# Kernel tuning notes

Hardware: AMD Instinct MI355X
Metric: run time of the kernel (lower is better)

Reference implementation:

```python
import jax, jax.numpy as jnp
import numpy as np
from jax import lax

DIVISOR = 2.0
POOL = 2

def setup_inputs() -> dict:
    key = jax.random.key(0)
    k1, k2, k3, k4 = jax.random.split(key, 4)
    x = jax.random.normal(k1, (16, 8, 16, 128, 128), dtype=jnp.float32)
    conv_weight = jax.random.normal(k2, (32, 8, 3, 3, 3), dtype=jnp.float32) * 0.05
    conv_bias = jax.random.normal(k3, (32,), dtype=jnp.float32) * 0.05
    bias = jax.random.normal(k4, (32, 1, 1, 1), dtype=jnp.float32)
    return {"x": x, "conv_weight": conv_weight, "conv_bias": conv_bias, "bias": bias}

def reference(x, conv_weight, conv_bias, bias):
    # Conv3d, valid padding, stride 1: [B,Cin,D,H,W] -> [B,Cout,D-2,H-2,W-2]
    y = lax.conv_general_dilated(
        x, conv_weight,
        window_strides=(1, 1, 1), padding="VALID",
        dimension_numbers=("NCDHW", "OIDHW", "NCDHW"))
    y = y + conv_bias[None, :, None, None, None]
    y = y / DIVISOR
    # MaxPool3d(2): non-overlapping 2x2x2 windows, floor mode
    y = lax.reduce_window(
        y, -jnp.inf, lax.max,
        window_dimensions=(1, 1, POOL, POOL, POOL),
        window_strides=(1, 1, POOL, POOL, POOL),
        padding="VALID")
    # AdaptiveAvgPool3d((1,1,1)) -> [B,C,1,1,1]
    y = jnp.mean(y, axis=(2, 3, 4), keepdims=True)
    # bias add (C,1,1,1) then sum over channel dim (sum_dim=1)
    y = y + bias
    return jnp.sum(y, axis=1)  # [B,1,1,1]
```

## Files before the change

kernel.cpp:

```cpp
#include <hip/hip_runtime.h>
#include <math.h>

namespace {

constexpr int B = 16, CIN = 8, D = 16, H = 128, W = 128;
constexpr int PW = 63;
constexpr float INV_CNT = 1.0f / 27783.0f;
constexpr int HW = H * W, DHW = D * HW;

typedef short v8s  __attribute__((ext_vector_type(8)));
typedef float v16f __attribute__((ext_vector_type(16)));

constexpr int WB_OFF = 131072;
constexpr int RED_OFF = WB_OFF + 14336;
constexpr int LDS_BYTES = RED_OFF + 64;

__device__ inline unsigned short f2bf(float f) {
    unsigned int x = __builtin_bit_cast(unsigned int, f);
    return (unsigned short)((x + 0x7FFFu + ((x >> 16) & 1u)) >> 16);
}

__global__ __launch_bounds__(512, 2) void conv_mfma_kernel(
    const float* __restrict__ x,
    const float* __restrict__ wgt,
    const float* __restrict__ cbias,
    float* __restrict__ partials)
{
    __shared__ __align__(16) char smem[LDS_BYTES];

    const int bid = blockIdx.x;
    const int logical = (bid & 7) * 126 + (bid >> 3);
    const int ph = logical % 63;
    const int b  = logical / 63;

    const int t = threadIdx.x, lane = t & 63, wv = t >> 6;

    for (int pr = t; pr < 14 * 64; pr += 512) {
        const int p = pr >> 6, l = pr & 63;
        const int tap = 2 * p + (l >> 5), cout = l & 31;
        uint4 pk = {0u, 0u, 0u, 0u};
        if (tap < 27) {
            unsigned int v[4];
            #pragma unroll
            for (int j = 0; j < 4; ++j) {
                unsigned short b0 = f2bf(wgt[(cout * CIN + 2 * j) * 27 + tap]);
                unsigned short b1 = f2bf(wgt[(cout * CIN + 2 * j + 1) * 27 + tap]);
                v[j] = (unsigned int)b0 | ((unsigned int)b1 << 16);
            }
            pk = uint4{v[0], v[1], v[2], v[3]};
        }
        *reinterpret_cast<uint4*>(smem + WB_OFF + pr * 16) = pk;
    }

    const float* xb = x + (size_t)b * CIN * DHW;
    #pragma unroll 4
    for (int s = t; s < 8192; s += 512) {
        const int d = s >> 9, h = (s >> 7) & 3, w = s & 127;
        const float* xp = xb + d * HW + (2 * ph + h) * W + w;
        unsigned int v[4];
        #pragma unroll
        for (int j = 0; j < 4; ++j) {
            unsigned short b0 = f2bf(xp[(2 * j) * DHW]);
            unsigned short b1 = f2bf(xp[(2 * j + 1) * DHW]);
            v[j] = (unsigned int)b0 | ((unsigned int)b1 << 16);
        }
        const int byte = (s * 16) ^ ((h & 1) << 6);
        *reinterpret_cast<uint4*>(smem + byte) = uint4{v[0], v[1], v[2], v[3]};
    }

    __syncthreads();

    v8s Bf[14];
    #pragma unroll
    for (int ks = 0; ks < 14; ++ks)
        Bf[ks] = *reinterpret_cast<const v8s*>(smem + WB_OFF + (ks * 64 + lane) * 16);

    const int r = lane & 31, half = lane >> 5;
    const int hh = r >> 4, pwl = (r >> 1) & 7, ww = r & 1;
    const int wbase = 2 * (8 * wv + pwl) + ww;

    int offA[14];
    #pragma unroll
    for (int ks = 0; ks < 14; ++ks) {
        const int t0 = 2 * ks, t1 = t0 + 1;
        const int KD0 = t0 / 9, KH0 = (t0 % 9) / 3, KW0 = t0 % 3;
        const int KD1 = (t1 < 27) ? t1 / 9 : 0;
        const int KH1 = (t1 < 27) ? (t1 % 9) / 3 : 0;
        const int KW1 = (t1 < 27) ? t1 % 3 : 0;
        const int kd = half ? KD1 : KD0;
        const int kh = half ? KH1 : KH0;
        const int kw = half ? KW1 : KW0;
        const int h = hh + kh;
        int w = wbase + kw; w = (w > 127) ? 127 : w;
        offA[ks] = (((kd * 4 + h) * 128 + w) * 16) ^ ((h & 1) << 6);
    }

    const float cb = cbias[lane & 31];
    float lsum = 0.f;

    #pragma unroll 1
    for (int pd = 0; pd < 7; ++pd) {
        v16f acc0, acc1;
        #pragma unroll
        for (int i = 0; i < 16; ++i) { acc0[i] = 0.f; acc1[i] = 0.f; }
        const int pbase = pd * 16384;

        #pragma unroll
        for (int ks = 0; ks < 14; ++ks) {
            const v8s A0 = *reinterpret_cast<const v8s*>(smem + pbase + offA[ks]);
            const v8s A1 = *reinterpret_cast<const v8s*>(smem + pbase + offA[ks] + 8192);
            acc0 = __builtin_amdgcn_mfma_f32_32x32x16_bf16(A0, Bf[ks], acc0, 0, 0, 0);
            acc1 = __builtin_amdgcn_mfma_f32_32x32x16_bf16(A1, Bf[ks], acc1, 0, 0, 0);
        }

        #pragma unroll
        for (int j = 0; j < 4; ++j) {
            float m = fmaxf(fmaxf(acc0[2 * j], acc0[2 * j + 1]),
                            fmaxf(acc0[8 + 2 * j], acc0[9 + 2 * j]));
            m = fmaxf(m, fmaxf(fmaxf(acc1[2 * j], acc1[2 * j + 1]),
                               fmaxf(acc1[8 + 2 * j], acc1[9 + 2 * j])));
            const int pw = 8 * wv + ((j & 1) + ((j >> 1) << 2) + 2 * half);
            if (pw < PW) lsum += (m + cb) * 0.5f;
        }
    }

    #pragma unroll
    for (int o = 32; o > 0; o >>= 1) lsum += __shfl_xor(lsum, o, 64);
    if (lane == 0) *reinterpret_cast<float*>(smem + RED_OFF + wv * 4) = lsum;
    __syncthreads();
    if (t == 0) {
        float s = 0.f;
        #pragma unroll
        for (int i = 0; i < 8; ++i) s += reinterpret_cast<float*>(smem + RED_OFF)[i];
        partials[logical] = s;
    }
}

__global__ void finalize_kernel(const float* __restrict__ partials,
                                const float* __restrict__ bias,
                                float* __restrict__ out)
{
    const int t = threadIdx.x;
    const int b = t >> 5, l = t & 31;
    float s = 0.f;
    for (int j = l; j < 63; j += 32) s += partials[b * 63 + j];
    s = s * INV_CNT + bias[l];
    #pragma unroll
    for (int o = 16; o > 0; o >>= 1) s += __shfl_xor(s, o, 32);
    if (l == 0) out[b] = s;
}

}

extern "C" void kernel_launch(void* const* d_in, const int* in_sizes, int n_in,
                              void* d_out, int out_size, void* d_ws, size_t ws_size,
                              hipStream_t stream) {
    const float* x     = (const float*)d_in[0];
    const float* wgt   = (const float*)d_in[1];
    const float* cbias = (const float*)d_in[2];
    const float* bias  = (const float*)d_in[3];
    float* out      = (float*)d_out;
    float* partials = (float*)d_ws;

    hipLaunchKernelGGL(conv_mfma_kernel, dim3(B * 63), dim3(512), 0, stream,
                       x, wgt, cbias, partials);
    hipLaunchKernelGGL(finalize_kernel, dim3(1), dim3(512), 0, stream,
                       partials, bias, out);
}
```

Baseline: 242.9 us.

## Split depth pairs across waves and overlap input staging with MFMA compute

Each wave pair now splits the two depth slices of a pooled output row, and the conv tile is remapped so each wave covers a 32-wide w strip. Partial maxima are exchanged through a double-buffered LDS area. Only the first six input planes are staged before compute starts; the remaining planes are staged two at a time inside the depth loop, so global loads overlap with MFMA work. This drops the XOR swizzle and adds a block barrier per iteration, which may bring back LDS bank conflicts and synchronisation cost.

```diff
diff --git a/kernel.cpp b/kernel.cpp
--- a/kernel.cpp
+++ b/kernel.cpp
@@ -4,20 +4,37 @@
 namespace {
 
 constexpr int B = 16, CIN = 8, D = 16, H = 128, W = 128;
-constexpr int PW = 63;
 constexpr float INV_CNT = 1.0f / 27783.0f;
 constexpr int HW = H * W, DHW = D * HW;
 
 typedef short v8s  __attribute__((ext_vector_type(8)));
 typedef float v16f __attribute__((ext_vector_type(16)));
 
-constexpr int WB_OFF = 131072;
-constexpr int RED_OFF = WB_OFF + 14336;
+constexpr int WB_OFF  = 131072;
+constexpr int PM_OFF  = WB_OFF + 14336;
+constexpr int RED_OFF = PM_OFF + 16384;
 constexpr int LDS_BYTES = RED_OFF + 64;
 
 __device__ inline unsigned short f2bf(float f) {
     unsigned int x = __builtin_bit_cast(unsigned int, f);
     return (unsigned short)((x + 0x7FFFu + ((x >> 16) & 1u)) >> 16);
+}
+
+__device__ inline void stage_planes(char* smem, const float* xb, int ph,
+                                    int dlo, int nplanes, int t) {
+    for (int s = t; s < nplanes * 512; s += 512) {
+        const int d = dlo + (s >> 9), h = (s >> 7) & 3, w = s & 127;
+        const float* xp = xb + d * HW + (2 * ph + h) * W + w;
+        unsigned int v[4];
+        #pragma unroll
+        for (int j = 0; j < 4; ++j) {
+            unsigned short b0 = f2bf(xp[(2 * j) * DHW]);
+            unsigned short b1 = f2bf(xp[(2 * j + 1) * DHW]);
+            v[j] = (unsigned int)b0 | ((unsigned int)b1 << 16);
+        }
+        *reinterpret_cast<uint4*>(smem + ((d * 4 + h) * 128 + w) * 16) =
+            uint4{v[0], v[1], v[2], v[3]};
+    }
 }
 
 __global__ __launch_bounds__(512, 2) void conv_mfma_kernel(
@@ -34,6 +51,8 @@
     const int b  = logical / 63;
 
     const int t = threadIdx.x, lane = t & 63, wv = t >> 6;
+    const int dd = wv & 1, q = wv >> 1, w0 = 32 * q;
+    const int r = lane & 31, half = lane >> 5;
 
     for (int pr = t; pr < 14 * 64; pr += 512) {
         const int p = pr >> 6, l = pr & 63;
@@ -53,21 +72,7 @@
     }
 
     const float* xb = x + (size_t)b * CIN * DHW;
-    #pragma unroll 4
-    for (int s = t; s < 8192; s += 512) {
-        const int d = s >> 9, h = (s >> 7) & 3, w = s & 127;
-        const float* xp = xb + d * HW + (2 * ph + h) * W + w;
-        unsigned int v[4];
-        #pragma unroll
-        for (int j = 0; j < 4; ++j) {
-            unsigned short b0 = f2bf(xp[(2 * j) * DHW]);
-            unsigned short b1 = f2bf(xp[(2 * j + 1) * DHW]);
-            v[j] = (unsigned int)b0 | ((unsigned int)b1 << 16);
-        }
-        const int byte = (s * 16) ^ ((h & 1) << 6);
-        *reinterpret_cast<uint4*>(smem + byte) = uint4{v[0], v[1], v[2], v[3]};
-    }
-
+    stage_planes(smem, xb, ph, 0, 6, t);
     __syncthreads();
 
     v8s Bf[14];
@@ -75,24 +80,12 @@
     for (int ks = 0; ks < 14; ++ks)
         Bf[ks] = *reinterpret_cast<const v8s*>(smem + WB_OFF + (ks * 64 + lane) * 16);
 
-    const int r = lane & 31, half = lane >> 5;
-    const int hh = r >> 4, pwl = (r >> 1) & 7, ww = r & 1;
-    const int wbase = 2 * (8 * wv + pwl) + ww;
-
     int offA[14];
     #pragma unroll
     for (int ks = 0; ks < 14; ++ks) {
-        const int t0 = 2 * ks, t1 = t0 + 1;
-        const int KD0 = t0 / 9, KH0 = (t0 % 9) / 3, KW0 = t0 % 3;
-        const int KD1 = (t1 < 27) ? t1 / 9 : 0;
-        const int KH1 = (t1 < 27) ? (t1 % 9) / 3 : 0;
-        const int KW1 = (t1 < 27) ? t1 % 3 : 0;
-        const int kd = half ? KD1 : KD0;
-        const int kh = half ? KH1 : KH0;
-        const int kw = half ? KW1 : KW0;
-        const int h = hh + kh;
-        int w = wbase + kw; w = (w > 127) ? 127 : w;
-        offA[ks] = (((kd * 4 + h) * 128 + w) * 16) ^ ((h & 1) << 6);
+        int tap = 2 * ks + half; if (tap > 26) tap = 26;
+        const int kd = tap / 9, kh = (tap % 9) / 3, kw = tap % 3;
+        offA[ks] = kd * 8192 + kh * 2048 + (w0 + r + kw) * 16;
     }
 
     const float cb = cbias[lane & 31];
@@ -103,35 +96,52 @@
         v16f acc0, acc1;
         #pragma unroll
         for (int i = 0; i < 16; ++i) { acc0[i] = 0.f; acc1[i] = 0.f; }
-        const int pbase = pd * 16384;
+        const int cbase = (2 * pd + dd) * 8192;
 
         #pragma unroll
         for (int ks = 0; ks < 14; ++ks) {
-            const v8s A0 = *reinterpret_cast<const v8s*>(smem + pbase + offA[ks]);
-            const v8s A1 = *reinterpret_cast<const v8s*>(smem + pbase + offA[ks] + 8192);
+            const v8s A0 = *reinterpret_cast<const v8s*>(smem + cbase + offA[ks]);
+            const v8s A1 = *reinterpret_cast<const v8s*>(smem + cbase + offA[ks] + 2048);
             acc0 = __builtin_amdgcn_mfma_f32_32x32x16_bf16(A0, Bf[ks], acc0, 0, 0, 0);
             acc1 = __builtin_amdgcn_mfma_f32_32x32x16_bf16(A1, Bf[ks], acc1, 0, 0, 0);
         }
 
+        float pm[8];
         #pragma unroll
-        for (int j = 0; j < 4; ++j) {
-            float m = fmaxf(fmaxf(acc0[2 * j], acc0[2 * j + 1]),
-                            fmaxf(acc0[8 + 2 * j], acc0[9 + 2 * j]));
-            m = fmaxf(m, fmaxf(fmaxf(acc1[2 * j], acc1[2 * j + 1]),
-                               fmaxf(acc1[8 + 2 * j], acc1[9 + 2 * j])));
-            const int pw = 8 * wv + ((j & 1) + ((j >> 1) << 2) + 2 * half);
-            if (pw < PW) lsum += (m + cb) * 0.5f;
+        for (int i = 0; i < 8; ++i)
+            pm[i] = fmaxf(fmaxf(acc0[2 * i], acc0[2 * i + 1]),
+                          fmaxf(acc1[2 * i], acc1[2 * i + 1]));
+
+        char* pmbuf = smem + PM_OFF + (pd & 1) * 8192 + (q * 64 + lane) * 32;
+        if (dd == 1) {
+            *reinterpret_cast<float4*>(pmbuf)      = float4{pm[0], pm[1], pm[2], pm[3]};
+            *reinterpret_cast<float4*>(pmbuf + 16) = float4{pm[4], pm[5], pm[6], pm[7]};
+        }
+        if (pd <= 4) stage_planes(smem, xb, ph, 2 * pd + 6, 2, t);
+        __syncthreads();
+
+        if (dd == 0) {
+            const float4 pa = *reinterpret_cast<const float4*>(pmbuf);
+            const float4 pb = *reinterpret_cast<const float4*>(pmbuf + 16);
+            const float pp[8] = {pa.x, pa.y, pa.z, pa.w, pb.x, pb.y, pb.z, pb.w};
+            #pragma unroll
+            for (int i = 0; i < 8; ++i) {
+                const int pw = 16 * q + (i & 1) + 4 * (i >> 1) + 2 * half;
+                const float m = fmaxf(pm[i], pp[i]);
+                if (pw < 63) lsum += (m + cb) * 0.5f;
+            }
         }
     }
 
     #pragma unroll
     for (int o = 32; o > 0; o >>= 1) lsum += __shfl_xor(lsum, o, 64);
-    if (lane == 0) *reinterpret_cast<float*>(smem + RED_OFF + wv * 4) = lsum;
+    if (dd == 0 && lane == 0)
+        reinterpret_cast<float*>(smem + RED_OFF)[q] = lsum;
     __syncthreads();
     if (t == 0) {
         float s = 0.f;
         #pragma unroll
-        for (int i = 0; i < 8; ++i) s += reinterpret_cast<float*>(smem + RED_OFF)[i];
+        for (int i = 0; i < 4; ++i) s += reinterpret_cast<float*>(smem + RED_OFF)[i];
         partials[logical] = s;
     }
 }
```

Measured after the change: 253.2 us. +4.2%, slower.

## Remap MFMA tiles to 32-wide W rows with four accumulators per wave

Applied to the files above, without the earlier changes.

Reassigns wave work so each wave handles 32 consecutive output W positions across both H rows and both D slices of a pool window, using four MFMA accumulators per step. Pooled-depth iterations are split between two wave halves. The LDS XOR swizzle is dropped, so A-fragment addressing becomes linear. The intent is more MFMA work per loop iteration and simpler address arithmetic, at the cost of higher accumulator register pressure, possible LDS bank conflicts, and load imbalance between the two depth halves (4 vs 3 iterations).

```diff
diff --git a/kernel.cpp b/kernel.cpp
--- a/kernel.cpp
+++ b/kernel.cpp
@@ -4,14 +4,13 @@
 namespace {
 
 constexpr int B = 16, CIN = 8, D = 16, H = 128, W = 128;
-constexpr int PW = 63;
 constexpr float INV_CNT = 1.0f / 27783.0f;
 constexpr int HW = H * W, DHW = D * HW;
 
 typedef short v8s  __attribute__((ext_vector_type(8)));
 typedef float v16f __attribute__((ext_vector_type(16)));
 
-constexpr int WB_OFF = 131072;
+constexpr int WB_OFF  = 131072;
 constexpr int RED_OFF = WB_OFF + 14336;
 constexpr int LDS_BYTES = RED_OFF + 64;
 
@@ -34,6 +33,8 @@
     const int b  = logical / 63;
 
     const int t = threadIdx.x, lane = t & 63, wv = t >> 6;
+    const int q = wv & 3, pdh = wv >> 2, w0 = 32 * q;
+    const int r = lane & 31, half = lane >> 5;
 
     for (int pr = t; pr < 14 * 64; pr += 512) {
         const int p = pr >> 6, l = pr & 63;
@@ -64,8 +65,7 @@
             unsigned short b1 = f2bf(xp[(2 * j + 1) * DHW]);
             v[j] = (unsigned int)b0 | ((unsigned int)b1 << 16);
         }
-        const int byte = (s * 16) ^ ((h & 1) << 6);
-        *reinterpret_cast<uint4*>(smem + byte) = uint4{v[0], v[1], v[2], v[3]};
+        *reinterpret_cast<uint4*>(smem + s * 16) = uint4{v[0], v[1], v[2], v[3]};
     }
 
     __syncthreads();
@@ -75,58 +75,54 @@
     for (int ks = 0; ks < 14; ++ks)
         Bf[ks] = *reinterpret_cast<const v8s*>(smem + WB_OFF + (ks * 64 + lane) * 16);
 
-    const int r = lane & 31, half = lane >> 5;
-    const int hh = r >> 4, pwl = (r >> 1) & 7, ww = r & 1;
-    const int wbase = 2 * (8 * wv + pwl) + ww;
-
     int offA[14];
     #pragma unroll
     for (int ks = 0; ks < 14; ++ks) {
-        const int t0 = 2 * ks, t1 = t0 + 1;
-        const int KD0 = t0 / 9, KH0 = (t0 % 9) / 3, KW0 = t0 % 3;
-        const int KD1 = (t1 < 27) ? t1 / 9 : 0;
-        const int KH1 = (t1 < 27) ? (t1 % 9) / 3 : 0;
-        const int KW1 = (t1 < 27) ? t1 % 3 : 0;
-        const int kd = half ? KD1 : KD0;
-        const int kh = half ? KH1 : KH0;
-        const int kw = half ? KW1 : KW0;
-        const int h = hh + kh;
-        int w = wbase + kw; w = (w > 127) ? 127 : w;
-        offA[ks] = (((kd * 4 + h) * 128 + w) * 16) ^ ((h & 1) << 6);
+        int tap = 2 * ks + half; if (tap > 26) tap = 26;
+        const int kd = tap / 9, kh = (tap % 9) / 3, kw = tap % 3;
+        int w = w0 + r + kw; if (w > 127) w = 127;
+        offA[ks] = kd * 8192 + kh * 2048 + w * 16;
     }
 
     const float cb = cbias[lane & 31];
+    const int pd0 = pdh ? 4 : 0;
+    const int npd = pdh ? 3 : 4;
     float lsum = 0.f;
 
     #pragma unroll 1
-    for (int pd = 0; pd < 7; ++pd) {
-        v16f acc0, acc1;
+    for (int pp = 0; pp < npd; ++pp) {
+        const int pbase = (pd0 + pp) * 16384;
+        v16f a00, a01, a10, a11;
         #pragma unroll
-        for (int i = 0; i < 16; ++i) { acc0[i] = 0.f; acc1[i] = 0.f; }
-        const int pbase = pd * 16384;
+        for (int i = 0; i < 16; ++i) { a00[i] = 0.f; a01[i] = 0.f; a10[i] = 0.f; a11[i] = 0.f; }
 
         #pragma unroll
         for (int ks = 0; ks < 14; ++ks) {
-            const v8s A0 = *reinterpret_cast<const v8s*>(smem + pbase + offA[ks]);
-            const v8s A1 = *reinterpret_cast<const v8s*>(smem + pbase + offA[ks] + 8192);
-            acc0 = __builtin_amdgcn_mfma_f32_32x32x16_bf16(A0, Bf[ks], acc0, 0, 0, 0);
-            acc1 = __builtin_amdgcn_mfma_f32_32x32x16_bf16(A1, Bf[ks], acc1, 0, 0, 0);
+            const char* base = smem + pbase + offA[ks];
+            const v8s A00 = *reinterpret_cast<const v8s*>(base);
+            const v8s A10 = *reinterpret_cast<const v8s*>(base + 2048);
+            const v8s A01 = *reinterpret_cast<const v8s*>(base + 8192);
+            const v8s A11 = *reinterpret_cast<const v8s*>(base + 10240);
+            a00 = __builtin_amdgcn_mfma_f32_32x32x16_bf16(A00, Bf[ks], a00, 0, 0, 0);
+            a10 = __builtin_amdgcn_mfma_f32_32x32x16_bf16(A10, Bf[ks], a10, 0, 0, 0);
+            a01 = __builtin_amdgcn_mfma_f32_32x32x16_bf16(A01, Bf[ks], a01, 0, 0, 0);
+            a11 = __builtin_amdgcn_mfma_f32_32x32x16_bf16(A11, Bf[ks], a11, 0, 0, 0);
         }
 
         #pragma unroll
-        for (int j = 0; j < 4; ++j) {
-            float m = fmaxf(fmaxf(acc0[2 * j], acc0[2 * j + 1]),
-                            fmaxf(acc0[8 + 2 * j], acc0[9 + 2 * j]));
-            m = fmaxf(m, fmaxf(fmaxf(acc1[2 * j], acc1[2 * j + 1]),
-                               fmaxf(acc1[8 + 2 * j], acc1[9 + 2 * j])));
-            const int pw = 8 * wv + ((j & 1) + ((j >> 1) << 2) + 2 * half);
-            if (pw < PW) lsum += (m + cb) * 0.5f;
+        for (int j = 0; j < 8; ++j) {
+            float m = fmaxf(fmaxf(a00[2 * j], a00[2 * j + 1]),
+                            fmaxf(a10[2 * j], a10[2 * j + 1]));
+            m = fmaxf(m, fmaxf(fmaxf(a01[2 * j], a01[2 * j + 1]),
+                               fmaxf(a11[2 * j], a11[2 * j + 1])));
+            const int pw = 16 * q + (j & 1) + 4 * (j >> 1) + 2 * half;
+            if (pw < 63) lsum += (m + cb) * 0.5f;
         }
     }
 
     #pragma unroll
     for (int o = 32; o > 0; o >>= 1) lsum += __shfl_xor(lsum, o, 64);
-    if (lane == 0) *reinterpret_cast<float*>(smem + RED_OFF + wv * 4) = lsum;
+    if (lane == 0) reinterpret_cast<float*>(smem + RED_OFF)[wv] = lsum;
     __syncthreads();
     if (t == 0) {
         float s = 0.f;
```

Result: no change. 239.7 us (-1.3%).
